# Kernel optimization log

Measured on AMD Instinct MI355X. Metric: run time of the kernel, lower is better.

## Reference

```python
import jax, jax.numpy as jnp
import numpy as np

N_NODES = 50000
N_EDGES = 1600000
IN_DIM = 1024
HID = 128
N_GRAPHS = 64


def setup_inputs() -> dict:
    key = jax.random.key(0)
    ks = jax.random.split(key, 8)
    x = jax.random.normal(ks[0], (N_NODES, IN_DIM), dtype=jnp.float32)
    edge_index = jax.random.randint(ks[1], (2, N_EDGES), 0, N_NODES, dtype=jnp.int32)
    batch = jnp.sort(jax.random.randint(ks[2], (N_NODES,), 0, N_GRAPHS, dtype=jnp.int32))
    # GATConv parameters (single head, concat irrelevant for 1 head)
    glorot = 1.0 / np.sqrt(IN_DIM)
    W = jax.random.uniform(ks[3], (IN_DIM, HID), minval=-glorot, maxval=glorot, dtype=jnp.float32)
    ga = 1.0 / np.sqrt(HID)
    att_src = jax.random.uniform(ks[4], (HID,), minval=-ga, maxval=ga, dtype=jnp.float32)
    att_dst = jax.random.uniform(ks[5], (HID,), minval=-ga, maxval=ga, dtype=jnp.float32)
    bias = jnp.zeros((HID,), dtype=jnp.float32)
    return {"x": x, "W": W, "att_src": att_src, "att_dst": att_dst, "bias": bias,
            "edge_index": edge_index, "batch": batch, "num_graphs": N_GRAPHS}


def reference(x, W, att_src, att_dst, bias, edge_index, batch, num_graphs):
    N = x.shape[0]
    h = x @ W                               # [N, HID]
    # add self-loops (GATConv default add_self_loops=True)
    loops = jnp.arange(N, dtype=edge_index.dtype)
    src = jnp.concatenate([edge_index[0], loops])   # [E+N]
    dst = jnp.concatenate([edge_index[1], loops])
    a_src = h @ att_src                     # [N]
    a_dst = h @ att_dst                     # [N]
    e = jax.nn.leaky_relu(a_src[src] + a_dst[dst], negative_slope=0.2)  # [E+N]
    # scatter-softmax over incoming edges of each destination node
    m = jax.ops.segment_max(e, dst, num_segments=N)
    p = jnp.exp(e - m[dst])
    denom = jax.ops.segment_sum(p, dst, num_segments=N)
    alpha = p / denom[dst]                  # [E+N]
    # attention-weighted aggregation
    out = jax.ops.segment_sum(alpha[:, None] * h[src], dst, num_segments=N)  # [N, HID]
    out = jax.nn.relu(out + bias)
    # global max pool over graphs in the batch
    return jax.ops.segment_max(out, batch, num_segments=num_graphs)          # [G, HID]
```

## Files before the change

kernel.cpp:

```cpp
#include <hip/hip_runtime.h>
#include <hip/hip_bf16.h>

#define N_NODES 50000
#define N_EDGES 1600000
#define IN_DIM 1024
#define HID 128
#define AGG_WAVES 6144

typedef __bf16 bf16x8 __attribute__((ext_vector_type(8)));
typedef float f32x4 __attribute__((ext_vector_type(4)));
typedef __bf16 bf16x4 __attribute__((ext_vector_type(4)));

__device__ __forceinline__ float2 bf2f(unsigned u) {
    return make_float2(__uint_as_float(u << 16), __uint_as_float(u & 0xffff0000u));
}
__device__ __forceinline__ float lrelu(float v) { return v > 0.f ? v : 0.2f * v; }

__global__ void prep_kernel(const float* __restrict__ W, __bf16* __restrict__ wt,
                            int* __restrict__ deg, float* __restrict__ out, int out_n) {
    int i = blockIdx.x * 256 + threadIdx.x;
    if (i < N_NODES) deg[i] = 0;
    if (i < out_n) out[i] = 0.0f;
    if (i < HID * IN_DIM) {
        int n = i >> 10, k = i & 1023;
        wt[i] = (__bf16)W[(size_t)k * HID + n];
    }
}

__global__ __launch_bounds__(256) void gemm_kernel(const float* __restrict__ x,
                                                   const __bf16* __restrict__ wt,
                                                   __bf16* __restrict__ h2,
                                                   const float* __restrict__ att_s,
                                                   const float* __restrict__ att_d,
                                                   float* __restrict__ o_as,
                                                   float* __restrict__ o_ad) {
    __shared__ __bf16 xa[64][40];
    __shared__ __bf16 wb[128][40];
    const int t = threadIdx.x;
    const int m0 = blockIdx.x * 64;
    const int wid = t >> 6, lane = t & 63;
    const int lm = lane & 15, q8 = (lane >> 4) * 8;
    const int rw0 = wid * 16;

    const int xrow = t >> 2, xkq = (t & 3);
    const int wn = t >> 1, wc2 = (t & 1);

    float4 xs_reg[2];
    uint2  ws_reg[4];

    auto stage_regs = [&](int k0) {
#pragma unroll
        for (int l = 0; l < 2; ++l) {
            int f = t + l * 256;
            int row = f >> 3, kq = f & 7;
            int gr = m0 + row;
            float4 v = make_float4(0.f, 0.f, 0.f, 0.f);
            if (gr < N_NODES)
                v = *(const float4*)(x + (size_t)gr * IN_DIM + k0 + kq * 4);
            xs_reg[l] = v;
        }
#pragma unroll
        for (int l = 0; l < 4; ++l) {
            int f = t + l * 256;
            int n = f >> 3, c = f & 7;
            ws_reg[l] = *(const uint2*)(wt + (size_t)n * IN_DIM + k0 + c * 4);
        }
    };
    auto regs_to_lds = [&]() {
#pragma unroll
        for (int l = 0; l < 2; ++l) {
            int f = t + l * 256;
            int row = f >> 3, kq = f & 7;
            bf16x4 b;
            b[0] = (__bf16)xs_reg[l].x; b[1] = (__bf16)xs_reg[l].y;
            b[2] = (__bf16)xs_reg[l].z; b[3] = (__bf16)xs_reg[l].w;
            *(bf16x4*)&xa[row][kq * 4] = b;
        }
#pragma unroll
        for (int l = 0; l < 4; ++l) {
            int f = t + l * 256;
            int n = f >> 3, c = f & 7;
            *(uint2*)&wb[n][c * 4] = ws_reg[l];
        }
    };

    f32x4 acc[8] = {};
    stage_regs(0);
    regs_to_lds();
    __syncthreads();
    for (int it = 0; it < 32; ++it) {
        if (it + 1 < 32) stage_regs((it + 1) * 32);
        bf16x8 af = *(const bf16x8*)&xa[rw0 + lm][q8];
#pragma unroll
        for (int ct = 0; ct < 8; ++ct) {
            bf16x8 bfr = *(const bf16x8*)&wb[ct * 16 + lm][q8];
            acc[ct] = __builtin_amdgcn_mfma_f32_16x16x32_bf16(af, bfr, acc[ct], 0, 0, 0);
        }
        if (it + 1 < 32) {
            __syncthreads();
            regs_to_lds();
            __syncthreads();
        }
    }
    const int quad = lane >> 4;
    float attsf[8], attdf[8];
#pragma unroll
    for (int ct = 0; ct < 8; ++ct) {
        attsf[ct] = att_s[ct * 16 + lm];
        attdf[ct] = att_d[ct * 16 + lm];
    }
#pragma unroll
    for (int reg = 0; reg < 4; ++reg) {
        int row = m0 + rw0 + quad * 4 + reg;
        float ps = 0.f, pd = 0.f;
#pragma unroll
        for (int ct = 0; ct < 8; ++ct) {
            float v = acc[ct][reg];
            ps = fmaf(v, attsf[ct], ps);
            pd = fmaf(v, attdf[ct], pd);
        }
#pragma unroll
        for (int o = 8; o; o >>= 1) {
            ps += __shfl_xor(ps, o);
            pd += __shfl_xor(pd, o);
        }
        if (row < N_NODES) {
            if (lm == 0) { o_as[row] = ps; o_ad[row] = pd; }
#pragma unroll
            for (int ct = 0; ct < 8; ++ct)
                h2[(size_t)row * HID + ct * 16 + lm] = (__bf16)acc[ct][reg];
        }
    }
    (void)xrow; (void)xkq; (void)wn; (void)wc2;
}

__global__ void hist_kernel(const int* __restrict__ ei, int* __restrict__ deg) {
    int e = blockIdx.x * 256 + threadIdx.x;
    if (e < N_EDGES) atomicAdd(&deg[ei[N_EDGES + e]], 1);
}

__global__ void scan1_kernel(const int* __restrict__ deg, int* __restrict__ bsum) {
    int b = blockIdx.x, t = threadIdx.x;
    int base = b * 1024 + t * 4;
    int s = 0;
#pragma unroll
    for (int j = 0; j < 4; ++j) {
        int idx = base + j;
        if (idx < N_NODES) s += deg[idx];
    }
    for (int o = 32; o; o >>= 1) s += __shfl_xor(s, o);
    __shared__ int wsum[4];
    int lane = t & 63, w = t >> 6;
    if (lane == 0) wsum[w] = s;
    __syncthreads();
    if (t == 0) bsum[b] = wsum[0] + wsum[1] + wsum[2] + wsum[3];
}

__global__ void scan2_kernel(const int* __restrict__ bsum, int* __restrict__ boff,
                             int* __restrict__ rowstart, int nb) {
    if (threadIdx.x == 0 && blockIdx.x == 0) {
        int run = 0;
        for (int i = 0; i < nb; ++i) { boff[i] = run; run += bsum[i]; }
        rowstart[N_NODES] = run;
    }
}

__global__ void scan3_kernel(int* __restrict__ deg, const int* __restrict__ boff,
                             int* __restrict__ rowstart) {
    int b = blockIdx.x, t = threadIdx.x;
    int base = b * 1024 + t * 4;
    int v[4]; int s = 0;
#pragma unroll
    for (int j = 0; j < 4; ++j) {
        int idx = base + j;
        v[j] = (idx < N_NODES) ? deg[idx] : 0;
        s += v[j];
    }
    int lane = t & 63, w = t >> 6;
    int inc = s;
    for (int o = 1; o < 64; o <<= 1) {
        int u = __shfl_up(inc, o);
        if (lane >= o) inc += u;
    }
    __shared__ int wt[4];
    if (lane == 63) wt[w] = inc;
    __syncthreads();
    int woff = 0;
    for (int i = 0; i < w; ++i) woff += wt[i];
    int run = woff + inc - s + boff[b];
#pragma unroll
    for (int j = 0; j < 4; ++j) {
        int idx = base + j;
        if (idx < N_NODES) {
            rowstart[idx] = run;
            run += v[j];
            deg[idx] = 0;
        }
    }
}

__global__ void scatter_kernel(const int* __restrict__ ei, const int* __restrict__ rowstart,
                               int* __restrict__ cursor, uint2* __restrict__ csrp,
                               const float* __restrict__ a_src) {
    int e = blockIdx.x * 256 + threadIdx.x;
    if (e >= N_EDGES) return;
    int s = ei[e], d = ei[N_EDGES + e];
    int pos = atomicAdd(&cursor[d], 1);
    uint2 v; v.x = (unsigned)s; v.y = __float_as_uint(a_src[s]);
    csrp[rowstart[d] + pos] = v;
}

__global__ __launch_bounds__(256, 6) void aggregate_kernel(
    const unsigned* __restrict__ h2u, const float* __restrict__ a_src,
    const float* __restrict__ a_dst, const int* __restrict__ rowstart,
    const uint2* __restrict__ csrp, const float* __restrict__ bias,
    const int* __restrict__ batch, float* __restrict__ out) {
    const int wid = threadIdx.x >> 6, lane = threadIdx.x & 63;
    const int w = blockIdx.x * 4 + wid;
    const int q = N_NODES / AGG_WAVES;
    const int r = N_NODES - q * AGG_WAVES;
    int n0 = w * q + (w < r ? w : r);
    int n1 = n0 + q + (w < r ? 1 : 0);
    const float b0 = bias[2 * lane], b1 = bias[2 * lane + 1];

    int gcur = -1;
    float m0 = 0.f, m1 = 0.f;
    for (int n = n0; n < n1; ++n) {
        int rs = rowstart[n], re = rowstart[n + 1];
        float adn = a_dst[n];
        float pself = __expf(lrelu(a_src[n] + adn));
        float2 hv = bf2f(h2u[(size_t)n * 64 + lane]);
        float denom = pself;
        float2 acc = make_float2(pself * hv.x, pself * hv.y);
        for (int base = rs; base < re; base += 64) {
            int cnt = re - base; if (cnt > 64) cnt = 64;
            uint2 sp = make_uint2(0u, 0u);
            bool valid = (base + lane < re);
            if (valid) sp = csrp[base + lane];
            float pe = valid ? __expf(lrelu(__uint_as_float(sp.y) + adn)) : 0.f;
            float ds = pe;
            for (int o = 32; o; o >>= 1) ds += __shfl_xor(ds, o);
            denom += ds;
            for (int e = 0; e < cnt; e += 16) {
                unsigned uu[16]; float pp[16];
#pragma unroll
                for (int i = 0; i < 16; ++i) {
                    unsigned src = (unsigned)__shfl((int)sp.x, e + i);
                    pp[i] = __shfl(pe, e + i);
                    uu[i] = h2u[(size_t)src * 64 + lane];
                }
#pragma unroll
                for (int i = 0; i < 16; ++i) {
                    float2 g = bf2f(uu[i]);
                    acc.x = fmaf(pp[i], g.x, acc.x);
                    acc.y = fmaf(pp[i], g.y, acc.y);
                }
            }
        }
        float inv = 1.0f / denom;
        float o0 = fmaxf(acc.x * inv + b0, 0.0f);
        float o1 = fmaxf(acc.y * inv + b1, 0.0f);
        int g = batch[n];
        if (g != gcur) {
            if (gcur >= 0) {
                unsigned* outp = (unsigned*)(out + (size_t)gcur * HID);
                atomicMax(&outp[2 * lane], __float_as_uint(m0));
                atomicMax(&outp[2 * lane + 1], __float_as_uint(m1));
            }
            gcur = g; m0 = o0; m1 = o1;
        } else {
            m0 = fmaxf(m0, o0); m1 = fmaxf(m1, o1);
        }
    }
    if (gcur >= 0) {
        unsigned* outp = (unsigned*)(out + (size_t)gcur * HID);
        atomicMax(&outp[2 * lane], __float_as_uint(m0));
        atomicMax(&outp[2 * lane + 1], __float_as_uint(m1));
    }
}

extern "C" void kernel_launch(void* const* d_in, const int* in_sizes, int n_in,
                              void* d_out, int out_size, void* d_ws, size_t ws_size,
                              hipStream_t stream) {
    const float* x     = (const float*)d_in[0];
    const float* W     = (const float*)d_in[1];
    const float* att_s = (const float*)d_in[2];
    const float* att_d = (const float*)d_in[3];
    const float* bias  = (const float*)d_in[4];
    const int*   ei    = (const int*)d_in[5];
    const int*   batch = (const int*)d_in[6];
    float*       out   = (float*)d_out;

    char* ws = (char*)d_ws;
    size_t off = 0;
    auto alloc = [&](size_t bytes) -> void* {
        void* p = ws + off;
        off += (bytes + 255) & ~(size_t)255;
        return p;
    };
    const int NB = (N_NODES + 1023) / 1024;
    __bf16* h2       = (__bf16*)alloc((size_t)N_NODES * HID * 2);
    __bf16* wt       = (__bf16*)alloc((size_t)HID * IN_DIM * 2);
    float*  a_src    = (float*)alloc((size_t)N_NODES * 4);
    float*  a_dst    = (float*)alloc((size_t)N_NODES * 4);
    int*    deg      = (int*)alloc((size_t)N_NODES * 4);
    int*    rowstart = (int*)alloc((size_t)(N_NODES + 1) * 4);
    int*    bsum     = (int*)alloc((size_t)NB * 4);
    int*    boff     = (int*)alloc((size_t)NB * 4);
    uint2*  csrp     = (uint2*)alloc((size_t)N_EDGES * 8);
    (void)ws_size; (void)in_sizes; (void)n_in;

    hipLaunchKernelGGL(prep_kernel, dim3(512), dim3(256), 0, stream,
                       W, wt, deg, out, out_size);
    hipLaunchKernelGGL(gemm_kernel, dim3((N_NODES + 63) / 64), dim3(256), 0, stream,
                       x, wt, h2, att_s, att_d, a_src, a_dst);
    hipLaunchKernelGGL(hist_kernel, dim3((N_EDGES + 255) / 256), dim3(256), 0, stream,
                       ei, deg);
    hipLaunchKernelGGL(scan1_kernel, dim3(NB), dim3(256), 0, stream, deg, bsum);
    hipLaunchKernelGGL(scan2_kernel, dim3(1), dim3(64), 0, stream, bsum, boff, rowstart, NB);
    hipLaunchKernelGGL(scan3_kernel, dim3(NB), dim3(256), 0, stream, deg, boff, rowstart);
    hipLaunchKernelGGL(scatter_kernel, dim3((N_EDGES + 255) / 256), dim3(256), 0, stream,
                       ei, rowstart, deg, csrp, a_src);
    hipLaunchKernelGGL(aggregate_kernel, dim3(AGG_WAVES / 4), dim3(256), 0, stream,
                       (const unsigned*)h2, a_src, a_dst, rowstart, csrp, bias, batch, out);
}
```

Before: 540.1 us.

## Double-buffer GEMM LDS tiles and reuse histogram atomic slots in scatter

The GEMM now keeps two LDS buffers for the x and W tiles, so the next tile is written into the alternate buffer and only one barrier per k-step is needed instead of two. Separately, the histogram kernel records each edge's atomicAdd return value as its slot within the destination row. The scatter kernel reuses that slot instead of issuing a second atomic on a reset counter, which also removes the counter reset in scan3. This trades 6.4MB of extra epos traffic and double the GEMM LDS footprint for fewer atomics and barriers.

Result: faster. 507.5 us (-6.0%).

```diff
diff --git a/kernel.cpp b/kernel.cpp
--- a/kernel.cpp
+++ b/kernel.cpp
@@ -34,16 +34,13 @@
                                                    const float* __restrict__ att_d,
                                                    float* __restrict__ o_as,
                                                    float* __restrict__ o_ad) {
-    __shared__ __bf16 xa[64][40];
-    __shared__ __bf16 wb[128][40];
+    __shared__ __bf16 xa[2][64][40];
+    __shared__ __bf16 wb[2][128][40];
     const int t = threadIdx.x;
     const int m0 = blockIdx.x * 64;
     const int wid = t >> 6, lane = t & 63;
     const int lm = lane & 15, q8 = (lane >> 4) * 8;
     const int rw0 = wid * 16;
-
-    const int xrow = t >> 2, xkq = (t & 3);
-    const int wn = t >> 1, wc2 = (t & 1);
 
     float4 xs_reg[2];
     uint2  ws_reg[4];
@@ -66,39 +63,39 @@
             ws_reg[l] = *(const uint2*)(wt + (size_t)n * IN_DIM + k0 + c * 4);
         }
     };
-    auto regs_to_lds = [&]() {
+    auto regs_to_lds = [&](int b) {
 #pragma unroll
         for (int l = 0; l < 2; ++l) {
             int f = t + l * 256;
             int row = f >> 3, kq = f & 7;
-            bf16x4 b;
-            b[0] = (__bf16)xs_reg[l].x; b[1] = (__bf16)xs_reg[l].y;
-            b[2] = (__bf16)xs_reg[l].z; b[3] = (__bf16)xs_reg[l].w;
-            *(bf16x4*)&xa[row][kq * 4] = b;
+            bf16x4 v;
+            v[0] = (__bf16)xs_reg[l].x; v[1] = (__bf16)xs_reg[l].y;
+            v[2] = (__bf16)xs_reg[l].z; v[3] = (__bf16)xs_reg[l].w;
+            *(bf16x4*)&xa[b][row][kq * 4] = v;
         }
 #pragma unroll
         for (int l = 0; l < 4; ++l) {
             int f = t + l * 256;
             int n = f >> 3, c = f & 7;
-            *(uint2*)&wb[n][c * 4] = ws_reg[l];
+            *(uint2*)&wb[b][n][c * 4] = ws_reg[l];
         }
     };
 
     f32x4 acc[8] = {};
     stage_regs(0);
-    regs_to_lds();
+    regs_to_lds(0);
     __syncthreads();
     for (int it = 0; it < 32; ++it) {
+        const int cur = it & 1;
         if (it + 1 < 32) stage_regs((it + 1) * 32);
-        bf16x8 af = *(const bf16x8*)&xa[rw0 + lm][q8];
+        bf16x8 af = *(const bf16x8*)&xa[cur][rw0 + lm][q8];
 #pragma unroll
         for (int ct = 0; ct < 8; ++ct) {
-            bf16x8 bfr = *(const bf16x8*)&wb[ct * 16 + lm][q8];
+            bf16x8 bfr = *(const bf16x8*)&wb[cur][ct * 16 + lm][q8];
             acc[ct] = __builtin_amdgcn_mfma_f32_16x16x32_bf16(af, bfr, acc[ct], 0, 0, 0);
         }
         if (it + 1 < 32) {
-            __syncthreads();
-            regs_to_lds();
+            regs_to_lds(cur ^ 1);
             __syncthreads();
         }
     }
@@ -131,12 +128,12 @@
                 h2[(size_t)row * HID + ct * 16 + lm] = (__bf16)acc[ct][reg];
         }
     }
-    (void)xrow; (void)xkq; (void)wn; (void)wc2;
-}
-
-__global__ void hist_kernel(const int* __restrict__ ei, int* __restrict__ deg) {
+}
+
+__global__ void hist_kernel(const int* __restrict__ ei, int* __restrict__ deg,
+                            int* __restrict__ epos) {
     int e = blockIdx.x * 256 + threadIdx.x;
-    if (e < N_EDGES) atomicAdd(&deg[ei[N_EDGES + e]], 1);
+    if (e < N_EDGES) epos[e] = atomicAdd(&deg[ei[N_EDGES + e]], 1);
 }
 
 __global__ void scan1_kernel(const int* __restrict__ deg, int* __restrict__ bsum) {
@@ -165,7 +162,7 @@
     }
 }
 
-__global__ void scan3_kernel(int* __restrict__ deg, const int* __restrict__ boff,
+__global__ void scan3_kernel(const int* __restrict__ deg, const int* __restrict__ boff,
                              int* __restrict__ rowstart) {
     int b = blockIdx.x, t = threadIdx.x;
     int base = b * 1024 + t * 4;
@@ -194,20 +191,18 @@
         if (idx < N_NODES) {
             rowstart[idx] = run;
             run += v[j];
-            deg[idx] = 0;
         }
     }
 }
 
 __global__ void scatter_kernel(const int* __restrict__ ei, const int* __restrict__ rowstart,
-                               int* __restrict__ cursor, uint2* __restrict__ csrp,
+                               const int* __restrict__ epos, uint2* __restrict__ csrp,
                                const float* __restrict__ a_src) {
     int e = blockIdx.x * 256 + threadIdx.x;
     if (e >= N_EDGES) return;
     int s = ei[e], d = ei[N_EDGES + e];
-    int pos = atomicAdd(&cursor[d], 1);
     uint2 v; v.x = (unsigned)s; v.y = __float_as_uint(a_src[s]);
-    csrp[rowstart[d] + pos] = v;
+    csrp[rowstart[d] + epos[e]] = v;
 }
 
 __global__ __launch_bounds__(256, 6) void aggregate_kernel(
@@ -307,6 +302,7 @@
     int*    rowstart = (int*)alloc((size_t)(N_NODES + 1) * 4);
     int*    bsum     = (int*)alloc((size_t)NB * 4);
     int*    boff     = (int*)alloc((size_t)NB * 4);
+    int*    epos     = (int*)alloc((size_t)N_EDGES * 4);
     uint2*  csrp     = (uint2*)alloc((size_t)N_EDGES * 8);
     (void)ws_size; (void)in_sizes; (void)n_in;
 
@@ -315,12 +311,12 @@
     hipLaunchKernelGGL(gemm_kernel, dim3((N_NODES + 63) / 64), dim3(256), 0, stream,
                        x, wt, h2, att_s, att_d, a_src, a_dst);
     hipLaunchKernelGGL(hist_kernel, dim3((N_EDGES + 255) / 256), dim3(256), 0, stream,
-                       ei, deg);
+                       ei, deg, epos);
     hipLaunchKernelGGL(scan1_kernel, dim3(NB), dim3(256), 0, stream, deg, bsum);
     hipLaunchKernelGGL(scan2_kernel, dim3(1), dim3(64), 0, stream, bsum, boff, rowstart, NB);
     hipLaunchKernelGGL(scan3_kernel, dim3(NB), dim3(256), 0, stream, deg, boff, rowstart);
     hipLaunchKernelGGL(scatter_kernel, dim3((N_EDGES + 255) / 256), dim3(256), 0, stream,
-                       ei, rowstart, deg, csrp, a_src);
+                       ei, rowstart, epos, csrp, a_src);
     hipLaunchKernelGGL(aggregate_kernel, dim3(AGG_WAVES / 4), dim3(256), 0, stream,
                        (const unsigned*)h2, a_src, a_dst, rowstart, csrp, bias, batch, out);
 }
```
